# Performance work log

Measured on AMD Instinct MI355X. Metric: run time of the kernel, lower is better.

Reference implementation:

```python
import jax, jax.numpy as jnp
import numpy as np

EPS = 1e-6
K = 20                 # k-NN neighbors (init default)
NEG_SLOPE_CONV = 0.2   # VNLinearLeakyReLU negative_slope in conv_pos / actvn_c
NEG_SLOPE_BLOCK = 0.0  # VNResnetBlockFC uses VNLeakyReLU(negative_slope=0.0)


def vn_linear(w, x):
    # w: [O, C], x: [B, C, 3, ...] -> [B, O, 3, ...]
    return jnp.einsum('oc,bc...->bo...', w, x)


def vn_leaky(x, d, slope):
    # Vector-neuron leaky ReLU: project onto learned direction d per channel.
    dot = jnp.sum(x * d, axis=2, keepdims=True)          # sum over 3-vector dim
    dsq = jnp.sum(d * d, axis=2, keepdims=True)
    x_neg = x - (dot / (dsq + EPS)) * d
    return slope * x + (1.0 - slope) * jnp.where(dot >= 0, x, x_neg)


def vn_lin_leaky(wf, wd, x, slope):
    return vn_leaky(vn_linear(wf, x), vn_linear(wd, x), slope)


def knn_idx(pts, k):
    # pts: [B, N, 3]; largest of negative squared distance = nearest (incl. self)
    d2 = jnp.sum(pts * pts, axis=-1)
    score = 2.0 * jnp.einsum('bnd,bmd->bnm', pts, pts) - d2[:, :, None] - d2[:, None, :]
    _, idx = jax.lax.top_k(score, k)
    return idx                                           # [B, N, k]


def graph_feature_cross(p, k):
    # p: [B, N, 3] -> edge features [B, 3(ch: rel, center, cross), 3(vec), N, k]
    idx = knn_idx(p, k)
    nb = jax.vmap(lambda pts, ix: pts[ix])(p, idx)       # [B, N, k, 3] gather
    ctr = jnp.broadcast_to(p[:, :, None, :], nb.shape)
    cross = jnp.cross(nb, ctr)
    feat = jnp.stack([nb - ctr, ctr, cross], axis=3)     # [B, N, k, 3ch, 3vec]
    return jnp.transpose(feat, (0, 3, 4, 1, 2))


def vn_resnet_block(x, wd0, wf0, wd1, wf1, wsc):
    net = vn_linear(wf0, vn_leaky(x, vn_linear(wd0, x), NEG_SLOPE_BLOCK))
    dx = vn_linear(wf1, vn_leaky(net, vn_linear(wd1, net), NEG_SLOPE_BLOCK))
    return vn_linear(wsc, x) + dx


def setup_inputs() -> dict:
    key = jax.random.key(0)
    ks = jax.random.split(key, 11)
    B, N = 4, 2048
    c_dim, hd = 128, 128
    s = lambda k_, sh, fan: (jax.random.normal(k_, sh, jnp.float32) / np.sqrt(fan).astype(np.float32))
    return {
        'p': jax.random.normal(ks[0], (B, N, 3), jnp.float32),
        'w_conv_feat': s(ks[1], (128, 3), 3),
        'w_conv_dir': s(ks[2], (128, 3), 3),
        'w_fc_pos': s(ks[3], (2 * hd, 128), 128),
        'blk_dir0': s(ks[4], (5, 2 * hd, 2 * hd), 2 * hd),
        'blk_fc0': s(ks[5], (5, hd, 2 * hd), 2 * hd),
        'blk_dir1': s(ks[6], (5, hd, hd), hd),
        'blk_fc1': s(ks[7], (5, hd, hd), hd),
        'blk_sc': s(ks[8], (5, hd, 2 * hd), 2 * hd),
        'w_actc_dir': s(ks[9], (hd, hd), hd),
        'w_fc_c': s(ks[10], (c_dim, hd), hd),
    }


def reference(p, w_conv_feat, w_conv_dir, w_fc_pos, blk_dir0, blk_fc0,
              blk_dir1, blk_fc1, blk_sc, w_actc_dir, w_fc_c):
    feat = graph_feature_cross(p, K)                     # [B, 3, 3, N, K]
    net = vn_lin_leaky(w_conv_feat, w_conv_dir, feat, NEG_SLOPE_CONV)
    net = net.mean(axis=-1)                              # pool over k -> [B,128,3,N]
    net = vn_linear(w_fc_pos, net)                       # [B,256,3,N]
    net = vn_resnet_block(net, blk_dir0[0], blk_fc0[0], blk_dir1[0], blk_fc1[0], blk_sc[0])
    for i in range(1, 5):                                # fixed 5-block stack
        pooled = jnp.broadcast_to(net.mean(axis=-1, keepdims=True), net.shape)
        net = jnp.concatenate([net, pooled], axis=1)     # [B,256,3,N]
        net = vn_resnet_block(net, blk_dir0[i], blk_fc0[i], blk_dir1[i], blk_fc1[i], blk_sc[i])
    net = net.mean(axis=-1)                              # global pool -> [B,128,3]
    net = vn_leaky(net, vn_linear(w_actc_dir, net), NEG_SLOPE_CONV)
    return vn_linear(w_fc_c, net)                        # c: [B,128,3]
```

## Files before the change

### kernel.cpp

```cpp
#include <hip/hip_runtime.h>
#include <math.h>

#define NPT 2048
#define BB 4
#define KNN 20
#define EPSV 1e-6f

typedef unsigned short u16;
typedef unsigned int u32;
typedef _Float16 half8 __attribute__((ext_vector_type(8)));
typedef __attribute__((ext_vector_type(4))) float f32x4;
typedef __attribute__((ext_vector_type(4))) u32 uint4v;

#define MFMAH(a,b,c) __builtin_amdgcn_mfma_f32_16x16x32_f16((a),(b),(c),0,0,0)

__device__ __forceinline__ u16 f2h(float f) {
    _Float16 h = (_Float16)f;
    return __builtin_bit_cast(u16, h);
}
__device__ __forceinline__ float h2f(u16 b) {
    return (float)__builtin_bit_cast(_Float16, b);
}

__global__ __launch_bounds__(256)
// ... 134 lines not shown
            a2 += 0.2f*fz + 0.8f*gz;
        }
        if (kh == 1) { part[o*3+0] = a0; part[o*3+1] = a1; part[o*3+2] = a2; }
        __syncthreads();
        if (kh == 0) {
            a0 += part[o*3+0]; a1 += part[o*3+1]; a2 += part[o*3+2];
            const float s = 1.f / (float)KNN;
            net1[(size_t)(b*6144 +          n)*128 + o] = f2h(a0*s);
            net1[(size_t)(b*6144 + 2048  + n)*128 + o] = f2h(a1*s);
            net1[(size_t)(b*6144 + 4096  + n)*128 + o] = f2h(a2*s);
        }
    }
}

template<int O, int C1, int C2, bool POOL, bool BIASED>
__global__ __launch_bounds__(256) void gemm_plain(
    const u16* __restrict__ W1, int ldw1,
    const u16* __restrict__ X1, int sx1,
    const u16* __restrict__ W2, int ldw2,
    const u16* __restrict__ X2, int sx2,
    const float* __restrict__ WscF, const float* __restrict__ PmPrev,
    u16* __restrict__ Y, int sy,
    float* __restrict__ PmOut)
{
    __shared__ __align__(16) char smem[64*132*4];
    __shared__ float pms[128];
    __shared__ float biasS_s[128];
    const int m0 = blockIdx.x * 64;
    const int ob = blockIdx.y * 128;
    const int b   = m0 / 6144;
    const int vec = (m0 % 6144) / 2048;
    const int tid = threadIdx.x;
    const int lane = tid & 63;
    const int wid = __builtin_amdgcn_readfirstlane(tid >> 6);
    const int wr = wid & 1, wc = wid >> 1;
    const int l15 = lane & 15, l4 = lane >> 4;

    if (BIASED) {
        if (tid < 128) pms[tid] = PmPrev[(size_t)(b*128 + tid)*3 + vec];
        __syncthreads();
        if (tid < 128) {
            const float* wrow = WscF + (size_t)tid*256 + 128;
            float s = 0.f;
            #pragma unroll 4
            for (int c = 0; c < 128; ++c) s += wrow[c]*pms[c];
            biasS_s[tid] = s;
        }
        __syncthreads();
    }

    f32x4 acc[4][2];
    #pragma unroll
    for (int io = 0; io < 4; ++io) {
        float bv[4];
        #pragma unroll
        for (int r = 0; r < 4; ++r)
            bv[r] = BIASED ? biasS_s[wr*64 + io*16 + l4*4 + r] : 0.f;
        #pragma unroll
        for (int jc = 0; jc < 2; ++jc)
            #pragma unroll
            for (int r = 0; r < 4; ++r) acc[io][jc][r] = bv[r];
    }

    constexpr int NS = (C1 + C2) / 64;
    auto ldaddr = [&](int st, int u) -> const u16* {
        const bool ph2 = (st >= C1/64);
        const u16* w = ph2 ? W2 : W1; const u16* x = ph2 ? X2 : X1;
        int ldw = ph2 ? ldw2 : ldw1; int sx = ph2 ? sx2 : sx1;
        int cc = (ph2 ? (st - C1/64) : st) * 64;
        if (u < 1024) {
            int row = u >> 3, q = u & 7;
            return w + (size_t)(ob + row)*ldw + cc + q*8;
        }
        int uu = u - 1024;
        int row = uu >> 3, q = uu & 7;
        return x + (size_t)(m0 + row)*sx + cc + q*8;
    };
    auto lds_dst = [&](int u) -> char* {
        if (u < 1024) { int row = u >> 3, q = u & 7; return smem + row*144 + q*16; }
        int uu = u - 1024;
        int row = uu >> 3, q = uu & 7;
        return smem + 18432 + row*144 + q*16;
    };

    uint4v pf[6];
    #pragma unroll
    for (int j = 0; j < 6; ++j) pf[j] = *reinterpret_cast<const uint4v*>(ldaddr(0, tid + 256*j));
    #pragma unroll
    for (int j = 0; j < 6; ++j) *reinterpret_cast<uint4v*>(lds_dst(tid + 256*j)) = pf[j];

    for (int st = 0; st < NS; ++st) {
        __syncthreads();
        if (st + 1 < NS) {
            #pragma unroll
            for (int j = 0; j < 6; ++j)
                pf[j] = *reinterpret_cast<const uint4v*>(ldaddr(st+1, tid + 256*j));
        }
        #pragma unroll
        for (int ks = 0; ks < 2; ++ks) {
            half8 fA[4], fB[2];
            #pragma unroll
            for (int io = 0; io < 4; ++io)
                fA[io] = *reinterpret_cast<const half8*>(smem + (wr*64 + io*16 + l15)*144 + ks*64 + l4*16);
            #pragma unroll
            for (int i = 0; i < 2; ++i)
                fB[i] = *reinterpret_cast<const half8*>(smem + 18432 + (wc*32 + i*16 + l15)*144 + ks*64 + l4*16);
            #pragma unroll
            for (int io = 0; io < 4; ++io)
                #pragma unroll
                for (int jc = 0; jc < 2; ++jc)
                    acc[io][jc] = MFMAH(fA[io], fB[jc], acc[io][jc]);
        }
        __syncthreads();
        if (st + 1 < NS) {
            #pragma unroll
            for (int j = 0; j < 6; ++j)
                *reinterpret_cast<uint4v*>(lds_dst(tid + 256*j)) = pf[j];
        }
    }

    float* sd = (float*)smem;
    #pragma unroll
    for (int io = 0; io < 4; ++io)
        #pragma unroll
        for (int jc = 0; jc < 2; ++jc) {
            int jj = wc*32 + jc*16 + l15;
            int orow = wr*64 + io*16 + l4*4;
            *reinterpret_cast<f32x4*>(sd + jj*132 + orow) = acc[io][jc];
        }
    __syncthreads();

    #pragma unroll
    for (int rep = 0; rep < 4; ++rep) {
        int task = tid + 256*rep;
        int oc = task & 15, ml = task >> 4;
        const float* dp = sd + ml*132 + oc*8;
        u32 hw[4];
        #pragma unroll
        for (int e2 = 0; e2 < 4; ++e2)
            hw[e2] = (u32)f2h(dp[2*e2]) | ((u32)f2h(dp[2*e2+1]) << 16);
        *reinterpret_cast<uint4v*>(Y + (size_t)(m0 + ml)*sy + ob + oc*8) =
            (uint4v){hw[0],hw[1],hw[2],hw[3]};
    }

    if (POOL) {
        int o_l = tid & 127, half = tid >> 7;
        float sum = 0.f;
        #pragma unroll 8
        for (int c = 0; c < 32; ++c) sum += sd[(half*32 + c)*132 + o_l];
        atomicAdd(&PmOut[(size_t)(b*128 + o_l)*3 + vec], sum * (1.f/(float)NPT));
    }
}

template<int O, int CIN, bool VIRT>
__global__ __launch_bounds__(256) void gemm_dir(
    const u16* __restrict__ W_, int ldw,
    const u16* __restrict__ X1, int sx,
    const float* __restrict__ WdF, const float* __restrict__ Pm,
    u16* __restrict__ Ov, int so,
    float* __restrict__ PmZero)
{
    __shared__ __align__(16) char smem[96*132*4];
    __shared__ float pmd[384];
    __shared__ float biasD_s[384];
    const int gx = blockIdx.x;
    const int b  = gx >> 6;
    const int n0 = (gx & 63) * 32;
    const int ob = blockIdx.y * 128;
    const int tid = threadIdx.x;
    const int lane = tid & 63;
    const int wid = __builtin_amdgcn_readfirstlane(tid >> 6);
    const int wr = wid & 1, wc = wid >> 1;
    const int l15 = lane & 15, l4 = lane >> 4;

    if (PmZero != nullptr && gx == 0 && blockIdx.y == 0)
        for (int t = tid; t < 1536; t += 256) PmZero[t] = 0.f;

    if (VIRT) {
        for (int t = tid; t < 384; t += 256) pmd[t] = Pm[(size_t)b*384 + t];
        __syncthreads();
        for (int t = tid; t < 384; t += 256) {
            int o_l = t / 3, v = t - o_l*3;
            const float* wrow = WdF + (size_t)(ob + o_l)*256 + 128;
            float s = 0.f;
            #pragma unroll 4
            for (int c = 0; c < 128; ++c) s += wrow[c]*pmd[c*3 + v];
            biasD_s[t] = s;
        }
        __syncthreads();
    }

    f32x4 acc[4][3];
    #pragma unroll
    for (int io = 0; io < 4; ++io)
        #pragma unroll
        for (int jc = 0; jc < 3; ++jc) {
            int v = (wc*48 + jc*16) >> 5;
            #pragma unroll
            for (int r = 0; r < 4; ++r) {
                int o_l = wr*64 + io*16 + l4*4 + r;
                acc[io][jc][r] = VIRT ? biasD_s[o_l*3 + v] : 0.f;
            }
        }

    constexpr int NS = CIN / 64;
    auto ldaddr = [&](int st, int u) -> const u16* {
        int cc = st*64;
        if (u < 1024) {
            int row = u >> 3, q = u & 7;
            return W_ + (size_t)(ob + row)*ldw + cc + q*8;
        }
        int uu = u - 1024;
        int row = uu >> 3, q = uu & 7;
        int m = b*6144 + (row >> 5)*2048 + n0 + (row & 31);
        return X1 + (size_t)m*sx + cc + q*8;
    };
    auto lds_dst = [&](int u) -> char* {
        if (u < 1024) { int row = u >> 3, q = u & 7; return smem + row*144 + q*16; }
        int uu = u - 1024;
        int row = uu >> 3, q = uu & 7;
        return smem + 18432 + row*144 + q*16;
    };

    uint4v pf[7];
    #pragma unroll
    for (int j = 0; j < 7; ++j) pf[j] = *reinterpret_cast<const uint4v*>(ldaddr(0, tid + 256*j));
    #pragma unroll
    for (int j = 0; j < 7; ++j) *reinterpret_cast<uint4v*>(lds_dst(tid + 256*j)) = pf[j];

    for (int st = 0; st < NS; ++st) {
        __syncthreads();
        if (st + 1 < NS) {
            #pragma unroll
            for (int j = 0; j < 7; ++j)
                pf[j] = *reinterpret_cast<const uint4v*>(ldaddr(st+1, tid + 256*j));
        }
        #pragma unroll
        for (int ks = 0; ks < 2; ++ks) {
            half8 fA[4], fB[3];
            #pragma unroll
            for (int io = 0; io < 4; ++io)
                fA[io] = *reinterpret_cast<const half8*>(smem + (wr*64 + io*16 + l15)*144 + ks*64 + l4*16);
            #pragma unroll
            for (int i = 0; i < 3; ++i)
                fB[i] = *reinterpret_cast<const half8*>(smem + 18432 + (wc*48 + i*16 + l15)*144 + ks*64 + l4*16);
            #pragma unroll
            for (int io = 0; io < 4; ++io)
                #pragma unroll
                for (int jc = 0; jc < 3; ++jc)
                    acc[io][jc] = MFMAH(fA[io], fB[jc], acc[io][jc]);
        }
        __syncthreads();
        if (st + 1 < NS) {
            #pragma unroll
            for (int j = 0; j < 7; ++j)
                *reinterpret_cast<uint4v*>(lds_dst(tid + 256*j)) = pf[j];
        }
    }

    float* sd = (float*)smem;
    #pragma unroll
    for (int io = 0; io < 4; ++io)
        #pragma unroll
        for (int jc = 0; jc < 3; ++jc) {
            int jj = wc*48 + jc*16 + l15;
            int orow = wr*64 + io*16 + l4*4;
            *reinterpret_cast<f32x4*>(sd + jj*132 + orow) = acc[io][jc];
        }
    __syncthreads();

    #pragma unroll
    for (int rep = 0; rep < 2; ++rep) {
        int task = tid + 256*rep;
        int oc = task & 15, nl = (task >> 4) & 31;
        float d[3][8], x[3][8];
        #pragma unroll
        for (int v = 0; v < 3; ++v) {
            const float* dp = sd + (v*32 + nl)*132 + oc*8;
            #pragma unroll
            for (int e = 0; e < 8; ++e) d[v][e] = dp[e];
        }
        if (VIRT && ob != 0) {
            #pragma unroll
            for (int e = 0; e < 8; ++e) {
                int c = oc*8 + e;
                #pragma unroll
                for (int v = 0; v < 3; ++v)
                    x[v][e] = Pm[(size_t)(b*128 + c)*3 + v];
            }
        } else {
            #pragma unroll
            for (int v = 0; v < 3; ++v) {
                size_t m = (size_t)(b*6144 + v*2048 + n0 + nl);
                uint4v hx = *reinterpret_cast<const uint4v*>(X1 + m*sx + ob + oc*8);
                #pragma unroll
                for (int w = 0; w < 4; ++w) {
                    x[v][2*w]   = h2f((u16)(hx[w] & 0xffffu));
                    x[v][2*w+1] = h2f((u16)(hx[w] >> 16));
                }
            }
        }
        #pragma unroll
        for (int e = 0; e < 8; ++e) {
            float d0 = d[0][e], d1 = d[1][e], d2 = d[2][e];
            float dot = x[0][e]*d0 + x[1][e]*d1 + x[2][e]*d2;
            float dsq = d0*d0 + d1*d1 + d2*d2;
            float t = dot / (dsq + EPSV);
            if (dot < 0.f) { x[0][e] -= t*d0; x[1][e] -= t*d1; x[2][e] -= t*d2; }
        }
        #pragma unroll
        for (int v = 0; v < 3; ++v) {
            u32 hw[4];
            #pragma unroll
            for (int e2 = 0; e2 < 4; ++e2)
                hw[e2] = (u32)f2h(x[v][2*e2]) | ((u32)f2h(x[v][2*e2+1]) << 16);
            *reinterpret_cast<uint4v*>(Ov + (size_t)(b*6144 + v*2048 + n0 + nl)*so + ob + oc*8) =
                (uint4v){hw[0],hw[1],hw[2],hw[3]};
        }
    }
}

template<int CSC, bool VIRT>
__global__ __launch_bounds__(256) void fused_back(
    const u16* __restrict__ Wf0,
    const u16* __restrict__ Wd,
    const u16* __restrict__ Wf1,
    const u16* __restrict__ Wsc,
    const float* __restrict__ WsF,
    const u16* __restrict__ A_,
    const u16* __restrict__ Xs,
    const float* __restrict__ Pm,
    u16* __restrict__ Y,
    float* __restrict__ PmOut)
{
    __shared__ __align__(16) char smem[77568];
    __shared__ float pms[384];
    __shared__ float biasS_s[384];
    constexpr int T_OFF = 0;
    constexpr int U_OFF = 26112;
    constexpr int SW    = 52224;
    const int gx = blockIdx.x;
    const int b  = gx >> 6;
    const int n0 = (gx & 63) * 32;
    const int tid = threadIdx.x;
    const int lane = tid & 63;
    const int wid = __builtin_amdgcn_readfirstlane(tid >> 6);
    const int wr = wid & 1, wc = wid >> 1;
    const int l15 = lane & 15, l4 = lane >> 4;

    if (VIRT) {
        for (int t = tid; t < 384; t += 256) pms[t] = Pm[(size_t)b*384 + t];
        __syncthreads();
        for (int t = tid; t < 384; t += 256) {
            int o_l = t / 3, v = t - o_l*3;
            const float* wrow = WsF + (size_t)o_l*256 + 128;
            float s = 0.f;
            #pragma unroll 4
            for (int c = 0; c < 128; ++c) s += wrow[c]*pms[c*3 + v];
            biasS_s[t] = s;
        }
        __syncthreads();
    }

    uint4v pf[7];

    {
        f32x4 accT[4][3];
        #pragma unroll
        for (int io = 0; io < 4; ++io)
            #pragma unroll
            for (int jc = 0; jc < 3; ++jc)
                accT[io][jc] = (f32x4){0.f,0.f,0.f,0.f};

        auto ldA = [&](int st, int u) -> const u16* {
            int cc = st*64;
            if (u < 1024) { int row = u >> 3, q = u & 7; return Wf0 + (size_t)row*256 + cc + q*8; }
            int uu = u - 1024;
            int row = uu >> 3, q = uu & 7;
            int m = b*6144 + (row >> 5)*2048 + n0 + (row & 31);
            return A_ + (size_t)m*256 + cc + q*8;
        };
        auto stA = [&](int u) -> char* {
            if (u < 1024) { int row = u >> 3, q = u & 7; return smem + SW + row*144 + q*16; }
            int uu = u - 1024;
            int row = uu >> 3, q = uu & 7;
            return smem + T_OFF + row*144 + q*16;
        };

        #pragma unroll
        for (int j = 0; j < 7; ++j) pf[j] = *reinterpret_cast<const uint4v*>(ldA(0, tid + 256*j));
        #pragma unroll
        for (int j = 0; j < 7; ++j) *reinterpret_cast<uint4v*>(stA(tid + 256*j)) = pf[j];

        for (int st = 0; st < 4; ++st) {
            __syncthreads();
            if (st + 1 < 4) {
                #pragma unroll
                for (int j = 0; j < 7; ++j)
                    pf[j] = *reinterpret_cast<const uint4v*>(ldA(st+1, tid + 256*j));
            }
            #pragma unroll
            for (int ks = 0; ks < 2; ++ks) {
                half8 fA[4], fB[3];
                #pragma unroll
                for (int io = 0; io < 4; ++io)
                    fA[io] = *reinterpret_cast<const half8*>(smem + SW + (wr*64 + io*16 + l15)*144 + ks*64 + l4*16);
                #pragma unroll
                for (int i = 0; i < 3; ++i)
                    fB[i] = *reinterpret_cast<const half8*>(smem + T_OFF + (wc*48 + i*16 + l15)*144 + ks*64 + l4*16);
                #pragma unroll
                for (int io = 0; io < 4; ++io)
                    #pragma unroll
                    for (int jc = 0; jc < 3; ++jc)
                        accT[io][jc] = MFMAH(fA[io], fB[jc], accT[io][jc]);
            }
            __syncthreads();
            if (st + 1 < 4) {
                #pragma unroll
                for (int j = 0; j < 7; ++j)
                    *reinterpret_cast<uint4v*>(stA(tid + 256*j)) = pf[j];
            }
        }

        float* sdT = (float*)(smem + U_OFF);
        #pragma unroll
        for (int io = 0; io < 4; ++io)
            #pragma unroll
            for (int jc = 0; jc < 3; ++jc) {
                int jj = wc*48 + jc*16 + l15;
                int orow = wr*64 + io*16 + l4*4;
                *reinterpret_cast<f32x4*>(sdT + jj*132 + orow) = accT[io][jc];
            }
        __syncthreads();
        #pragma unroll
        for (int rep = 0; rep < 6; ++rep) {
            int task = tid + 256*rep;
            int oc = task & 15, cidx = task >> 4;
            const float* dp = sdT + cidx*132 + oc*8;
            u32 hw[4];
            #pragma unroll
            for (int e2 = 0; e2 < 4; ++e2)
                hw[e2] = (u32)f2h(dp[2*e2]) | ((u32)f2h(dp[2*e2+1]) << 16);
            *reinterpret_cast<uint4v*>(smem + T_OFF + cidx*272 + oc*16) =
                (uint4v){hw[0],hw[1],hw[2],hw[3]};
        }
        __syncthreads();
    }

    f32x4 accD[4][3];
    #pragma unroll
    for (int io = 0; io < 4; ++io)
        #pragma unroll
        for (int jc = 0; jc < 3; ++jc)
            accD[io][jc] = (f32x4){0.f,0.f,0.f,0.f};
    {
        auto ldW = [&](int st, int u) -> const u16* {
            int row = u >> 3, q = u & 7;
            return Wd + (size_t)row*128 + st*64 + q*8;
        };
        #pragma unroll
        for (int j = 0; j < 4; ++j) pf[j] = *reinterpret_cast<const uint4v*>(ldW(0, tid + 256*j));
        #pragma unroll
        for (int j = 0; j < 4; ++j) { int u = tid + 256*j; int row = u >> 3, q = u & 7;
            *reinterpret_cast<uint4v*>(smem + SW + row*144 + q*16) = pf[j]; }

        for (int st = 0; st < 2; ++st) {
            __syncthreads();
            if (st + 1 < 2) {
                #pragma unroll
                for (int j = 0; j < 4; ++j)
                    pf[j] = *reinterpret_cast<const uint4v*>(ldW(st+1, tid + 256*j));
            }
            #pragma unroll
            for (int ks = 0; ks < 2; ++ks) {
                half8 fA[4], fB[3];
                #pragma unroll
                for (int io = 0; io < 4; ++io)
                    fA[io] = *reinterpret_cast<const half8*>(smem + SW + (wr*64 + io*16 + l15)*144 + ks*64 + l4*16);
                #pragma unroll
                for (int i = 0; i < 3; ++i)
                    fB[i] = *reinterpret_cast<const half8*>(smem + T_OFF + (wc*48 + i*16 + l15)*272 + st*128 + ks*64 + l4*16);
                #pragma unroll
                for (int io = 0; io < 4; ++io)
                    #pragma unroll
                    for (int jc = 0; jc < 3; ++jc)
                        accD[io][jc] = MFMAH(fA[io], fB[jc], accD[io][jc]);
            }
            __syncthreads();
            if (st + 1 < 2) {
                #pragma unroll
                for (int j = 0; j < 4; ++j) { int u = tid + 256*j; int row = u >> 3, q = u & 7;
                    *reinterpret_cast<uint4v*>(smem + SW + row*144 + q*16) = pf[j]; }
            }
        }
    }

    {
        float* sdT = (float*)(smem + U_OFF);
        #pragma unroll
        for (int io = 0; io < 4; ++io)
            #pragma unroll
            for (int jc = 0; jc < 3; ++jc) {
                int jj = wc*48 + jc*16 + l15;
                int orow = wr*64 + io*16 + l4*4;
                *reinterpret_cast<f32x4*>(sdT + jj*132 + orow) = accD[io][jc];
            }
        __syncthreads();
        #pragma unroll
        for (int rep = 0; rep < 2; ++rep) {
            int task = tid + 256*rep;
            int oc = task & 15, nl = task >> 4;
            float d[3][8], x[3][8];
            #pragma unroll
            for (int v = 0; v < 3; ++v) {
                const float* dp = sdT + (v*32 + nl)*132 + oc*8;
                #pragma unroll
                for (int e = 0; e < 8; ++e) d[v][e] = dp[e];
                uint4v hx = *reinterpret_cast<const uint4v*>(smem + T_OFF + (v*32 + nl)*272 + oc*16);
                #pragma unroll
                for (int w = 0; w < 4; ++w) {
                    x[v][2*w]   = h2f((u16)(hx[w] & 0xffffu));
                    x[v][2*w+1] = h2f((u16)(hx[w] >> 16));
                }
            }
            #pragma unroll
            for (int e = 0; e < 8; ++e) {
                float d0 = d[0][e], d1 = d[1][e], d2 = d[2][e];
                float dot = x[0][e]*d0 + x[1][e]*d1 + x[2][e]*d2;
                float dsq = d0*d0 + d1*d1 + d2*d2;
                float t = dot / (dsq + EPSV);
                if (dot < 0.f) { x[0][e] -= t*d0; x[1][e] -= t*d1; x[2][e] -= t*d2; }
            }
            #pragma unroll
            for (int v = 0; v < 3; ++v) {
                u32 hw[4];
                #pragma unroll
                for (int e2 = 0; e2 < 4; ++e2)
                    hw[e2] = (u32)f2h(x[v][2*e2]) | ((u32)f2h(x[v][2*e2+1]) << 16);
                *reinterpret_cast<uint4v*>(smem + T_OFF + (v*32 + nl)*272 + oc*16) =
                    (uint4v){hw[0],hw[1],hw[2],hw[3]};
            }
        }
        __syncthreads();
    }

    f32x4 acc2[4][3];
    #pragma unroll
    for (int io = 0; io < 4; ++io)
        #pragma unroll
        for (int jc = 0; jc < 3; ++jc) {
            int v = (wc*48 + jc*16) >> 5;
            #pragma unroll
            for (int r = 0; r < 4; ++r) {
                int o_l = wr*64 + io*16 + l4*4 + r;
                acc2[io][jc][r] = VIRT ? biasS_s[o_l*3 + v] : 0.f;
            }
        }

    constexpr int NS2 = 2 + CSC/64;
    auto ld2 = [&](int st, int u) -> const u16* {
        if (st < 2) {
            int row = u >> 3, q = u & 7;
            return Wf1 + (size_t)row*128 + st*64 + q*8;
        }
        int cc = (st - 2)*64;
        if (u < 1024) { int row = u >> 3, q = u & 7; return Wsc + (size_t)row*256 + cc + q*8; }
        int uu = u - 1024;
        int row = uu >> 3, q = uu & 7;
        int m = b*6144 + (row >> 5)*2048 + n0 + (row & 31);
        return Xs + (size_t)m*CSC + cc + q*8;
    };
    auto st2 = [&](int u) -> char* {
        if (u < 1024) { int row = u >> 3, q = u & 7; return smem + SW + row*144 + q*16; }
        int uu = u - 1024;
        int row = uu >> 3, q = uu & 7;
        return smem + U_OFF + row*144 + q*16;
    };

    #pragma unroll
    for (int j = 0; j < 7; ++j) { int u = tid + 256*j; if (u < 1024) pf[j] = *reinterpret_cast<const uint4v*>(ld2(0, u)); }
    #pragma unroll
    for (int j = 0; j < 7; ++j) { int u = tid + 256*j; if (u < 1024) *reinterpret_cast<uint4v*>(st2(u)) = pf[j]; }

    for (int st = 0; st < NS2; ++st) {
        __syncthreads();
        int nv = (st + 1 < 2) ? 1024 : 1792;
        if (st + 1 < NS2) {
            #pragma unroll
            for (int j = 0; j < 7; ++j) { int u = tid + 256*j; if (u < nv) pf[j] = *reinterpret_cast<const uint4v*>(ld2(st+1, u)); }
        }
        #pragma unroll
        for (int ks = 0; ks < 2; ++ks) {
            half8 fA[4], fB[3];
            #pragma unroll
            for (int io = 0; io < 4; ++io)
                fA[io] = *reinterpret_cast<const half8*>(smem + SW + (wr*64 + io*16 + l15)*144 + ks*64 + l4*16);
            if (st < 2) {
                #pragma unroll
                for (int i = 0; i < 3; ++i)
                    fB[i] = *reinterpret_cast<const half8*>(smem + T_OFF + (wc*48 + i*16 + l15)*272 + st*128 + ks*64 + l4*16);
            } else {
                #pragma unroll
                for (int i = 0; i < 3; ++i)
                    fB[i] = *reinterpret_cast<const half8*>(smem + U_OFF + (wc*48 + i*16 + l15)*144 + ks*64 + l4*16);
            }
            #pragma unroll
            for (int io = 0; io < 4; ++io)
                #pragma unroll
                for (int jc = 0; jc < 3; ++jc)
                    acc2[io][jc] = MFMAH(fA[io], fB[jc], acc2[io][jc]);
        }
        __syncthreads();
        if (st + 1 < NS2) {
            #pragma unroll
            for (int j = 0; j < 7; ++j) { int u = tid + 256*j; if (u < nv) *reinterpret_cast<uint4v*>(st2(u)) = pf[j]; }
        }
    }

    float* sdE = (float*)smem;
    #pragma unroll
    for (int io = 0; io < 4; ++io)
        #pragma unroll
        for (int jc = 0; jc < 3; ++jc) {
            int jj = wc*48 + jc*16 + l15;
            int orow = wr*64 + io*16 + l4*4;
            *reinterpret_cast<f32x4*>(sdE + jj*132 + orow) = acc2[io][jc];
        }
    __syncthreads();
    if (Y != nullptr) {
        #pragma unroll
        for (int rep = 0; rep < 2; ++rep) {
            int task = tid + 256*rep;
            int oc = task & 15, nl = (task >> 4) & 31;
            #pragma unroll
            for (int v = 0; v < 3; ++v) {
                const float* dp = sdE + (v*32 + nl)*132 + oc*8;
                u32 hw[4];
                #pragma unroll
                for (int e2 = 0; e2 < 4; ++e2)
                    hw[e2] = (u32)f2h(dp[2*e2]) | ((u32)f2h(dp[2*e2+1]) << 16);
                *reinterpret_cast<uint4v*>(Y + (size_t)(b*6144 + v*2048 + n0 + nl)*128 + oc*8) =
                    (uint4v){hw[0],hw[1],hw[2],hw[3]};
            }
        }
    }
    for (int t = tid; t < 384; t += 256) {
        int v = t >> 7, o_l = t & 127;
        float sum = 0.f;
        #pragma unroll 8
        for (int nl = 0; nl < 32; ++nl) sum += sdE[(v*32 + nl)*132 + o_l];
        atomicAdd(&PmOut[(size_t)(b*128 + o_l)*3 + v], sum * (1.f/(float)NPT));
    }
}

#define WO_FCPOS 0
#define WO_DIR0  32768
#define WO_FC0   360448
#define WO_DIR1  524288
#define WO_FC1   606208
#define WO_SC    688128
#define WTOT     851968
__global__ __launch_bounds__(256)
void convert_w_kernel(const float* __restrict__ s0, const float* __restrict__ s1,
                      const float* __restrict__ s2, const float* __restrict__ s3,
                      const float* __restrict__ s4, const float* __restrict__ s5,
                      u16* __restrict__ Wf) {
    int t = blockIdx.x*256 + threadIdx.x;
    if (t >= WTOT) return;
    const float* src; int base;
    if      (t < WO_DIR0) { src = s0; base = WO_FCPOS; }
    else if (t < WO_FC0)  { src = s1; base = WO_DIR0; }
    else if (t < WO_DIR1) { src = s2; base = WO_FC0; }
    else if (t < WO_FC1)  { src = s3; base = WO_DIR1; }
    else if (t < WO_SC)   { src = s4; base = WO_FC1; }
    else                  { src = s5; base = WO_SC; }
    Wf[t] = f2h(src[t - base]);
}

__global__ __launch_bounds__(128)
void final_head_kernel(const float* __restrict__ q, const float* __restrict__ Wdir,
                       const float* __restrict__ Wfc, float* __restrict__ out) {
    int b = blockIdx.x; int o = threadIdx.x;
    __shared__ float qs[128][3];
    __shared__ float zs[128][3];
    qs[o][0] = q[((size_t)b*128 + o)*3 + 0];
    qs[o][1] = q[((size_t)b*128 + o)*3 + 1];
    qs[o][2] = q[((size_t)b*128 + o)*3 + 2];
    __syncthreads();
    float d0 = 0.f, d1 = 0.f, d2 = 0.f;
    for (int c = 0; c < 128; ++c) {
        float w = Wdir[o*128 + c];
        d0 += w*qs[c][0]; d1 += w*qs[c][1]; d2 += w*qs[c][2];
    }
    float x0 = qs[o][0], x1 = qs[o][1], x2 = qs[o][2];
    float dot = d0*x0 + d1*x1 + d2*x2;
    float dsq = d0*d0 + d1*d1 + d2*d2;
    float t = dot / (dsq + EPSV);
    bool pos = dot >= 0.f;
    float g0 = pos ? x0 : (x0 - t*d0);
    float g1 = pos ? x1 : (x1 - t*d1);
    float g2 = pos ? x2 : (x2 - t*d2);
    zs[o][0] = 0.2f*x0 + 0.8f*g0;
    zs[o][1] = 0.2f*x1 + 0.8f*g1;
    zs[o][2] = 0.2f*x2 + 0.8f*g2;
    __syncthreads();
    float c0 = 0.f, c1 = 0.f, c2 = 0.f;
    for (int c = 0; c < 128; ++c) {
        float w = Wfc[o*128 + c];
        c0 += w*zs[c][0]; c1 += w*zs[c][1]; c2 += w*zs[c][2];
    }
    out[((size_t)b*128 + o)*3 + 0] = c0;
    out[((size_t)b*128 + o)*3 + 1] = c1;
    out[((size_t)b*128 + o)*3 + 2] = c2;
}

extern "C" void kernel_launch(void* const* d_in, const int* in_sizes, int n_in,
                              void* d_out, int out_size, void* d_ws, size_t ws_size,
                              hipStream_t stream) {
    const float* p           = (const float*)d_in[0];
    const float* w_conv_feat = (const float*)d_in[1];
    const float* w_conv_dir  = (const float*)d_in[2];
    const float* w_fc_pos    = (const float*)d_in[3];
    const float* blk_dir0    = (const float*)d_in[4];
    const float* blk_fc0     = (const float*)d_in[5];
    const float* blk_dir1    = (const float*)d_in[6];
    const float* blk_fc1     = (const float*)d_in[7];
    const float* blk_sc      = (const float*)d_in[8];
    const float* w_actc_dir  = (const float*)d_in[9];
    const float* w_fc_c      = (const float*)d_in[10];
    float* out = (float*)d_out;

    char* wsb = (char*)d_ws;
    size_t cur = 0;
    auto carve = [&](size_t nbytes) -> char* {
        char* r = wsb + cur;
        cur += (nbytes + 255) & ~(size_t)255;
        return r;
    };
    const size_t MTOT = (size_t)BB*3*NPT;
    float* Pm0   = (float*)carve(1536*4);
    float* Pm1   = (float*)carve(1536*4);
    u16* Wf    = (u16*)carve((size_t)WTOT*2);
    u16* net1  = (u16*)carve(MTOT*128*2);
    u16* X0    = (u16*)carve(MTOT*256*2);
    u16* Ab    = (u16*)carve(MTOT*256*2);
    u16* Yb    = (u16*)carve(MTOT*128*2);
    float* PmBuf[2] = { Pm0, Pm1 };

    convert_w_kernel<<<(WTOT+255)/256, 256, 0, stream>>>(
        w_fc_pos, blk_dir0, blk_fc0, blk_dir1, blk_fc1, blk_sc, Wf);
    knn_edge_kernel<<<BB*NPT, 256, 0, stream>>>(p, w_conv_feat, w_conv_dir, net1);

    gemm_plain<256,128,0,false,false><<<dim3(384,2), 256, 0, stream>>>(
        Wf+WO_FCPOS, 128, net1, 128,
        nullptr, 0, nullptr, 0,
        nullptr, nullptr, X0, 256, nullptr);

    const u16* Yp = nullptr;
    for (int i = 0; i < 5; ++i) {
        size_t od0 = WO_DIR0 + (size_t)i*65536;
        size_t of0 = WO_FC0  + (size_t)i*32768;
        size_t od1 = WO_DIR1 + (size_t)i*16384;
        size_t of1 = WO_FC1  + (size_t)i*16384;
        size_t osc = WO_SC   + (size_t)i*32768;
        float* PmPrev = PmBuf[(i+1) & 1];
        float* PmCur  = PmBuf[i & 1];

        if (i == 0) {
            gemm_dir<256,256,false><<<dim3(BB*64,2), 256, 0, stream>>>(
                Wf+od0, 256, X0, 256, nullptr, nullptr, Ab, 256, PmCur);
        } else {
            gemm_dir<256,128,true><<<dim3(BB*64,2), 256, 0, stream>>>(
                Wf+od0, 256, Yp, 128,
                blk_dir0 + (size_t)i*65536, PmPrev, Ab, 256, PmCur);
        }

        u16* outv = (i == 4) ? nullptr : ((i % 2 == 0) ? Yb : X0);
        if (i == 0) {
            fused_back<256,false><<<BB*64, 256, 0, stream>>>(
                Wf+of0, Wf+od1, Wf+of1, Wf+osc, nullptr,
                Ab, X0, nullptr, outv, PmCur);
        } else {
            fused_back<128,true><<<BB*64, 256, 0, stream>>>(
                Wf+of0, Wf+od1, Wf+of1, Wf+osc, blk_sc + (size_t)i*32768,
                Ab, Yp, PmPrev, outv, PmCur);
        }
        Yp = outv;
    }

    final_head_kernel<<<BB, 128, 0, stream>>>(PmBuf[0], w_actc_dir, w_fc_c, out);
}
```

Baseline: 288.6 us.

## Fuse direction GEMM and leaky ReLU into per-block resnet kernel

Result: slower. 311.3 us (+7.9%).

```diff
diff --git a/kernel.cpp b/kernel.cpp
--- a/kernel.cpp
+++ b/kernel.cpp
@@ -310,193 +310,28 @@
     }
 }
 
-template<int O, int CIN, bool VIRT>
-__global__ __launch_bounds__(256) void gemm_dir(
-    const u16* __restrict__ W_, int ldw,
-    const u16* __restrict__ X1, int sx,
-    const float* __restrict__ WdF, const float* __restrict__ Pm,
-    u16* __restrict__ Ov, int so,
-    float* __restrict__ PmZero)
-{
-    __shared__ __align__(16) char smem[96*132*4];
-    __shared__ float pmd[384];
-    __shared__ float biasD_s[384];
-    const int gx = blockIdx.x;
-    const int b  = gx >> 6;
-    const int n0 = (gx & 63) * 32;
-    const int ob = blockIdx.y * 128;
-    const int tid = threadIdx.x;
-    const int lane = tid & 63;
-    const int wid = __builtin_amdgcn_readfirstlane(tid >> 6);
-    const int wr = wid & 1, wc = wid >> 1;
-    const int l15 = lane & 15, l4 = lane >> 4;
-
-    if (PmZero != nullptr && gx == 0 && blockIdx.y == 0)
-        for (int t = tid; t < 1536; t += 256) PmZero[t] = 0.f;
-
-    if (VIRT) {
-        for (int t = tid; t < 384; t += 256) pmd[t] = Pm[(size_t)b*384 + t];
-        __syncthreads();
-        for (int t = tid; t < 384; t += 256) {
-            int o_l = t / 3, v = t - o_l*3;
-            const float* wrow = WdF + (size_t)(ob + o_l)*256 + 128;
-            float s = 0.f;
-            #pragma unroll 4
-            for (int c = 0; c < 128; ++c) s += wrow[c]*pmd[c*3 + v];
-            biasD_s[t] = s;
-        }
-        __syncthreads();
-    }
-
-    f32x4 acc[4][3];
-    #pragma unroll
-    for (int io = 0; io < 4; ++io)
-        #pragma unroll
-        for (int jc = 0; jc < 3; ++jc) {
-            int v = (wc*48 + jc*16) >> 5;
-            #pragma unroll
-            for (int r = 0; r < 4; ++r) {
-                int o_l = wr*64 + io*16 + l4*4 + r;
-                acc[io][jc][r] = VIRT ? biasD_s[o_l*3 + v] : 0.f;
-            }
-        }
-
-    constexpr int NS = CIN / 64;
-    auto ldaddr = [&](int st, int u) -> const u16* {
-        int cc = st*64;
-        if (u < 1024) {
-            int row = u >> 3, q = u & 7;
-            return W_ + (size_t)(ob + row)*ldw + cc + q*8;
-        }
-        int uu = u - 1024;
-        int row = uu >> 3, q = uu & 7;
-        int m = b*6144 + (row >> 5)*2048 + n0 + (row & 31);
-        return X1 + (size_t)m*sx + cc + q*8;
-    };
-    auto lds_dst = [&](int u) -> char* {
-        if (u < 1024) { int row = u >> 3, q = u & 7; return smem + row*144 + q*16; }
-        int uu = u - 1024;
-        int row = uu >> 3, q = uu & 7;
-        return smem + 18432 + row*144 + q*16;
-    };
-
-    uint4v pf[7];
-    #pragma unroll
-    for (int j = 0; j < 7; ++j) pf[j] = *reinterpret_cast<const uint4v*>(ldaddr(0, tid + 256*j));
-    #pragma unroll
-    for (int j = 0; j < 7; ++j) *reinterpret_cast<uint4v*>(lds_dst(tid + 256*j)) = pf[j];
-
-    for (int st = 0; st < NS; ++st) {
-        __syncthreads();
-        if (st + 1 < NS) {
-            #pragma unroll
-            for (int j = 0; j < 7; ++j)
-                pf[j] = *reinterpret_cast<const uint4v*>(ldaddr(st+1, tid + 256*j));
-        }
-        #pragma unroll
-        for (int ks = 0; ks < 2; ++ks) {
-            half8 fA[4], fB[3];
-            #pragma unroll
-            for (int io = 0; io < 4; ++io)
-                fA[io] = *reinterpret_cast<const half8*>(smem + (wr*64 + io*16 + l15)*144 + ks*64 + l4*16);
-            #pragma unroll
-            for (int i = 0; i < 3; ++i)
-                fB[i] = *reinterpret_cast<const half8*>(smem + 18432 + (wc*48 + i*16 + l15)*144 + ks*64 + l4*16);
-            #pragma unroll
-            for (int io = 0; io < 4; ++io)
-                #pragma unroll
-                for (int jc = 0; jc < 3; ++jc)
-                    acc[io][jc] = MFMAH(fA[io], fB[jc], acc[io][jc]);
-        }
-        __syncthreads();
-        if (st + 1 < NS) {
-            #pragma unroll
-            for (int j = 0; j < 7; ++j)
-                *reinterpret_cast<uint4v*>(lds_dst(tid + 256*j)) = pf[j];
-        }
-    }
-
-    float* sd = (float*)smem;
-    #pragma unroll
-    for (int io = 0; io < 4; ++io)
-        #pragma unroll
-        for (int jc = 0; jc < 3; ++jc) {
-            int jj = wc*48 + jc*16 + l15;
-            int orow = wr*64 + io*16 + l4*4;
-            *reinterpret_cast<f32x4*>(sd + jj*132 + orow) = acc[io][jc];
-        }
-    __syncthreads();
-
-    #pragma unroll
-    for (int rep = 0; rep < 2; ++rep) {
-        int task = tid + 256*rep;
-        int oc = task & 15, nl = (task >> 4) & 31;
-        float d[3][8], x[3][8];
-        #pragma unroll
-        for (int v = 0; v < 3; ++v) {
-            const float* dp = sd + (v*32 + nl)*132 + oc*8;
-            #pragma unroll
-            for (int e = 0; e < 8; ++e) d[v][e] = dp[e];
-        }
-        if (VIRT && ob != 0) {
-            #pragma unroll
-            for (int e = 0; e < 8; ++e) {
-                int c = oc*8 + e;
-                #pragma unroll
-                for (int v = 0; v < 3; ++v)
-                    x[v][e] = Pm[(size_t)(b*128 + c)*3 + v];
-            }
-        } else {
-            #pragma unroll
-            for (int v = 0; v < 3; ++v) {
-                size_t m = (size_t)(b*6144 + v*2048 + n0 + nl);
-                uint4v hx = *reinterpret_cast<const uint4v*>(X1 + m*sx + ob + oc*8);
-                #pragma unroll
-                for (int w = 0; w < 4; ++w) {
-                    x[v][2*w]   = h2f((u16)(hx[w] & 0xffffu));
-                    x[v][2*w+1] = h2f((u16)(hx[w] >> 16));
-                }
-            }
-        }
-        #pragma unroll
-        for (int e = 0; e < 8; ++e) {
-            float d0 = d[0][e], d1 = d[1][e], d2 = d[2][e];
-            float dot = x[0][e]*d0 + x[1][e]*d1 + x[2][e]*d2;
-            float dsq = d0*d0 + d1*d1 + d2*d2;
-            float t = dot / (dsq + EPSV);
-            if (dot < 0.f) { x[0][e] -= t*d0; x[1][e] -= t*d1; x[2][e] -= t*d2; }
-        }
-        #pragma unroll
-        for (int v = 0; v < 3; ++v) {
-            u32 hw[4];
-            #pragma unroll
-            for (int e2 = 0; e2 < 4; ++e2)
-                hw[e2] = (u32)f2h(x[v][2*e2]) | ((u32)f2h(x[v][2*e2+1]) << 16);
-            *reinterpret_cast<uint4v*>(Ov + (size_t)(b*6144 + v*2048 + n0 + nl)*so + ob + oc*8) =
-                (uint4v){hw[0],hw[1],hw[2],hw[3]};
-        }
-    }
-}
-
-template<int CSC, bool VIRT>
-__global__ __launch_bounds__(256) void fused_back(
+template<int CIN, bool VIRT>
+__global__ __launch_bounds__(256) void fused_iter(
+    const u16* __restrict__ Wd0,
+    const float* __restrict__ Wd0F,
     const u16* __restrict__ Wf0,
-    const u16* __restrict__ Wd,
+    const u16* __restrict__ Wd1,
     const u16* __restrict__ Wf1,
     const u16* __restrict__ Wsc,
     const float* __restrict__ WsF,
-    const u16* __restrict__ A_,
-    const u16* __restrict__ Xs,
+    const u16* __restrict__ Xin,
     const float* __restrict__ Pm,
     u16* __restrict__ Y,
     float* __restrict__ PmOut)
 {
-    __shared__ __align__(16) char smem[77568];
+    __shared__ __align__(16) char smem[76800];
     __shared__ float pms[384];
     __shared__ float biasS_s[384];
-    constexpr int T_OFF = 0;
-    constexpr int U_OFF = 26112;
-    constexpr int SW    = 52224;
+    __shared__ float biasD_s[384];
+    constexpr int R0  = 0;
+    constexpr int R1  = 26112;
+    constexpr int WST = R1;
+    constexpr int XST = R1 + 18432;
     const int gx = blockIdx.x;
     const int b  = gx >> 6;
     const int n0 = (gx & 63) * 32;
@@ -521,66 +356,198 @@
     }
 
     uint4v pf[7];
-
-    {
-        f32x4 accT[4][3];
+    f32x4 accT[4][3];
+    #pragma unroll
+    for (int io = 0; io < 4; ++io)
+        #pragma unroll
+        for (int jc = 0; jc < 3; ++jc)
+            accT[io][jc] = (f32x4){0.f,0.f,0.f,0.f};
+
+    for (int h = 0; h < 2; ++h) {
+        if (VIRT) {
+            __syncthreads();
+            for (int t = tid; t < 384; t += 256) {
+                int o_l = t / 3, v = t - o_l*3;
+                const float* wrow = Wd0F + (size_t)(h*128 + o_l)*256 + 128;
+                float s = 0.f;
+                #pragma unroll 4
+                for (int c = 0; c < 128; ++c) s += wrow[c]*pms[c*3 + v];
+                biasD_s[t] = s;
+            }
+            __syncthreads();
+        }
+
+        f32x4 accD0[4][3];
         #pragma unroll
         for (int io = 0; io < 4; ++io)
             #pragma unroll
-            for (int jc = 0; jc < 3; ++jc)
-                accT[io][jc] = (f32x4){0.f,0.f,0.f,0.f};
-
-        auto ldA = [&](int st, int u) -> const u16* {
+            for (int jc = 0; jc < 3; ++jc) {
+                int v = (wc*48 + jc*16) >> 5;
+                #pragma unroll
+                for (int r = 0; r < 4; ++r) {
+                    int o_l = wr*64 + io*16 + l4*4 + r;
+                    accD0[io][jc][r] = VIRT ? biasD_s[o_l*3 + v] : 0.f;
+                }
+            }
+
+        auto ldD = [&](int st, int u) -> const u16* {
             int cc = st*64;
-            if (u < 1024) { int row = u >> 3, q = u & 7; return Wf0 + (size_t)row*256 + cc + q*8; }
+            if (u < 1024) { int row = u >> 3, q = u & 7;
+                return Wd0 + (size_t)(h*128 + row)*256 + cc + q*8; }
             int uu = u - 1024;
             int row = uu >> 3, q = uu & 7;
             int m = b*6144 + (row >> 5)*2048 + n0 + (row & 31);
-            return A_ + (size_t)m*256 + cc + q*8;
+            return Xin + (size_t)m*CIN + cc + q*8;
         };
-        auto stA = [&](int u) -> char* {
-            if (u < 1024) { int row = u >> 3, q = u & 7; return smem + SW + row*144 + q*16; }
+        auto stD = [&](int u) -> char* {
+            if (u < 1024) { int row = u >> 3, q = u & 7; return smem + WST + row*144 + q*16; }
             int uu = u - 1024;
             int row = uu >> 3, q = uu & 7;
-            return smem + T_OFF + row*144 + q*16;
+            return smem + XST + row*144 + q*16;
         };
-
-        #pragma unroll
-        for (int j = 0; j < 7; ++j) pf[j] = *reinterpret_cast<const uint4v*>(ldA(0, tid + 256*j));
-        #pragma unroll
-        for (int j = 0; j < 7; ++j) *reinterpret_cast<uint4v*>(stA(tid + 256*j)) = pf[j];
-
-        for (int st = 0; st < 4; ++st) {
+        constexpr int NSD = CIN / 64;
+        #pragma unroll
+        for (int j = 0; j < 7; ++j) pf[j] = *reinterpret_cast<const uint4v*>(ldD(0, tid + 256*j));
+        #pragma unroll
+        for (int j = 0; j < 7; ++j) *reinterpret_cast<uint4v*>(stD(tid + 256*j)) = pf[j];
+        for (int st = 0; st < NSD; ++st) {
             __syncthreads();
-            if (st + 1 < 4) {
+            if (st + 1 < NSD) {
                 #pragma unroll
                 for (int j = 0; j < 7; ++j)
-                    pf[j] = *reinterpret_cast<const uint4v*>(ldA(st+1, tid + 256*j));
+                    pf[j] = *reinterpret_cast<const uint4v*>(ldD(st+1, tid + 256*j));
             }
             #pragma unroll
             for (int ks = 0; ks < 2; ++ks) {
                 half8 fA[4], fB[3];
                 #pragma unroll
                 for (int io = 0; io < 4; ++io)
-                    fA[io] = *reinterpret_cast<const half8*>(smem + SW + (wr*64 + io*16 + l15)*144 + ks*64 + l4*16);
+                    fA[io] = *reinterpret_cast<const half8*>(smem + WST + (wr*64 + io*16 + l15)*144 + ks*64 + l4*16);
                 #pragma unroll
                 for (int i = 0; i < 3; ++i)
-                    fB[i] = *reinterpret_cast<const half8*>(smem + T_OFF + (wc*48 + i*16 + l15)*144 + ks*64 + l4*16);
+                    fB[i] = *reinterpret_cast<const half8*>(smem + XST + (wc*48 + i*16 + l15)*144 + ks*64 + l4*16);
                 #pragma unroll
                 for (int io = 0; io < 4; ++io)
                     #pragma unroll
                     for (int jc = 0; jc < 3; ++jc)
-                        accT[io][jc] = MFMAH(fA[io], fB[jc], accT[io][jc]);
+                        accD0[io][jc] = MFMAH(fA[io], fB[jc], accD0[io][jc]);
             }
             __syncthreads();
-            if (st + 1 < 4) {
+            if (st + 1 < NSD) {
                 #pragma unroll
                 for (int j = 0; j < 7; ++j)
-                    *reinterpret_cast<uint4v*>(stA(tid + 256*j)) = pf[j];
-            }
-        }
-
-        float* sdT = (float*)(smem + U_OFF);
+                    *reinterpret_cast<uint4v*>(stD(tid + 256*j)) = pf[j];
+            }
+        }
+
+        {
+            float* sd = (float*)(smem + R1);
+            #pragma unroll
+            for (int io = 0; io < 4; ++io)
+                #pragma unroll
+                for (int jc = 0; jc < 3; ++jc) {
+                    int jj = wc*48 + jc*16 + l15;
+                    int orow = wr*64 + io*16 + l4*4;
+                    *reinterpret_cast<f32x4*>(sd + jj*132 + orow) = accD0[io][jc];
+                }
+            __syncthreads();
+            #pragma unroll
+            for (int rep = 0; rep < 2; ++rep) {
+                int task = tid + 256*rep;
+                int oc = task & 15, nl = task >> 4;
+                float d[3][8], x[3][8];
+                #pragma unroll
+                for (int v = 0; v < 3; ++v) {
+                    const float* dp = sd + (v*32 + nl)*132 + oc*8;
+                    #pragma unroll
+                    for (int e = 0; e < 8; ++e) d[v][e] = dp[e];
+                }
+                if (VIRT && h == 1) {
+                    #pragma unroll
+                    for (int e = 0; e < 8; ++e) {
+                        int c = oc*8 + e;
+                        #pragma unroll
+                        for (int v = 0; v < 3; ++v)
+                            x[v][e] = pms[c*3 + v];
+                    }
+                } else {
+                    #pragma unroll
+                    for (int v = 0; v < 3; ++v) {
+                        size_t m = (size_t)(b*6144 + v*2048 + n0 + nl);
+                        uint4v hx = *reinterpret_cast<const uint4v*>(
+                            Xin + m*CIN + (VIRT ? 0 : h*128) + oc*8);
+                        #pragma unroll
+                        for (int w = 0; w < 4; ++w) {
+                            x[v][2*w]   = h2f((u16)(hx[w] & 0xffffu));
+                            x[v][2*w+1] = h2f((u16)(hx[w] >> 16));
+                        }
+                    }
+                }
+                #pragma unroll
+                for (int e = 0; e < 8; ++e) {
+                    float d0 = d[0][e], d1 = d[1][e], d2 = d[2][e];
+                    float dot = x[0][e]*d0 + x[1][e]*d1 + x[2][e]*d2;
+                    float dsq = d0*d0 + d1*d1 + d2*d2;
+                    float t = dot / (dsq + EPSV);
+                    if (dot < 0.f) { x[0][e] -= t*d0; x[1][e] -= t*d1; x[2][e] -= t*d2; }
+                }
+                #pragma unroll
+                for (int v = 0; v < 3; ++v) {
+                    u32 hw[4];
+                    #pragma unroll
+                    for (int e2 = 0; e2 < 4; ++e2)
+                        hw[e2] = (u32)f2h(x[v][2*e2]) | ((u32)f2h(x[v][2*e2+1]) << 16);
+                    *reinterpret_cast<uint4v*>(smem + R0 + (v*32 + nl)*272 + oc*16) =
+                        (uint4v){hw[0],hw[1],hw[2],hw[3]};
+                }
+            }
+            __syncthreads();
+        }
+
+        {
+            auto ldF0 = [&](int st, int u) -> const u16* {
+                int row = u >> 3, q = u & 7;
+                return Wf0 + (size_t)row*256 + h*128 + st*64 + q*8;
+            };
+            #pragma unroll
+            for (int j = 0; j < 4; ++j) pf[j] = *reinterpret_cast<const uint4v*>(ldF0(0, tid + 256*j));
+            #pragma unroll
+            for (int j = 0; j < 4; ++j) { int u = tid + 256*j; int row = u >> 3, q = u & 7;
+                *reinterpret_cast<uint4v*>(smem + WST + row*144 + q*16) = pf[j]; }
+            for (int st = 0; st < 2; ++st) {
+                __syncthreads();
+                if (st + 1 < 2) {
+                    #pragma unroll
+                    for (int j = 0; j < 4; ++j)
+                        pf[j] = *reinterpret_cast<const uint4v*>(ldF0(st+1, tid + 256*j));
+                }
+                #pragma unroll
+                for (int ks = 0; ks < 2; ++ks) {
+                    half8 fA[4], fB[3];
+                    #pragma unroll
+                    for (int io = 0; io < 4; ++io)
+                        fA[io] = *reinterpret_cast<const half8*>(smem + WST + (wr*64 + io*16 + l15)*144 + ks*64 + l4*16);
+                    #pragma unroll
+                    for (int i = 0; i < 3; ++i)
+                        fB[i] = *reinterpret_cast<const half8*>(smem + R0 + (wc*48 + i*16 + l15)*272 + st*128 + ks*64 + l4*16);
+                    #pragma unroll
+                    for (int io = 0; io < 4; ++io)
+                        #pragma unroll
+                        for (int jc = 0; jc < 3; ++jc)
+                            accT[io][jc] = MFMAH(fA[io], fB[jc], accT[io][jc]);
+                }
+                __syncthreads();
+                if (st + 1 < 2) {
+                    #pragma unroll
+                    for (int j = 0; j < 4; ++j) { int u = tid + 256*j; int row = u >> 3, q = u & 7;
+                        *reinterpret_cast<uint4v*>(smem + WST + row*144 + q*16) = pf[j]; }
+                }
+            }
+        }
+    }
+
+    {
+        float* sdT = (float*)(smem + R1);
         #pragma unroll
         for (int io = 0; io < 4; ++io)
             #pragma unroll
@@ -599,7 +566,7 @@
             #pragma unroll
             for (int e2 = 0; e2 < 4; ++e2)
                 hw[e2] = (u32)f2h(dp[2*e2]) | ((u32)f2h(dp[2*e2+1]) << 16);
-            *reinterpret_cast<uint4v*>(smem + T_OFF + cidx*272 + oc*16) =
+            *reinterpret_cast<uint4v*>(smem + R0 + cidx*272 + oc*16) =
                 (uint4v){hw[0],hw[1],hw[2],hw[3]};
         }
         __syncthreads();
@@ -614,14 +581,13 @@
     {
         auto ldW = [&](int st, int u) -> const u16* {
             int row = u >> 3, q = u & 7;
-            return Wd + (size_t)row*128 + st*64 + q*8;
+            return Wd1 + (size_t)row*128 + st*64 + q*8;
         };
         #pragma unroll
         for (int j = 0; j < 4; ++j) pf[j] = *reinterpret_cast<const uint4v*>(ldW(0, tid + 256*j));
         #pragma unroll
         for (int j = 0; j < 4; ++j) { int u = tid + 256*j; int row = u >> 3, q = u & 7;
-            *reinterpret_cast<uint4v*>(smem + SW + row*144 + q*16) = pf[j]; }
-
+            *reinterpret_cast<uint4v*>(smem + WST + row*144 + q*16) = pf[j]; }
         for (int st = 0; st < 2; ++st) {
             __syncthreads();
             if (st + 1 < 2) {
@@ -634,10 +600,10 @@
                 half8 fA[4], fB[3];
                 #pragma unroll
                 for (int io = 0; io < 4; ++io)
-                    fA[io] = *reinterpret_cast<const half8*>(smem + SW + (wr*64 + io*16 + l15)*144 + ks*64 + l4*16);
+                    fA[io] = *reinterpret_cast<const half8*>(smem + WST + (wr*64 + io*16 + l15)*144 + ks*64 + l4*16);
                 #pragma unroll
                 for (int i = 0; i < 3; ++i)
-                    fB[i] = *reinterpret_cast<const half8*>(smem + T_OFF + (wc*48 + i*16 + l15)*272 + st*128 + ks*64 + l4*16);
+                    fB[i] = *reinterpret_cast<const half8*>(smem + R0 + (wc*48 + i*16 + l15)*272 + st*128 + ks*64 + l4*16);
                 #pragma unroll
                 for (int io = 0; io < 4; ++io)
                     #pragma unroll
@@ -648,13 +614,13 @@
             if (st + 1 < 2) {
                 #pragma unroll
                 for (int j = 0; j < 4; ++j) { int u = tid + 256*j; int row = u >> 3, q = u & 7;
-                    *reinterpret_cast<uint4v*>(smem + SW + row*144 + q*16) = pf[j]; }
+                    *reinterpret_cast<uint4v*>(smem + WST + row*144 + q*16) = pf[j]; }
             }
         }
     }
 
     {
-        float* sdT = (float*)(smem + U_OFF);
+        float* sdT = (float*)(smem + R1);
         #pragma unroll
         for (int io = 0; io < 4; ++io)
             #pragma unroll
@@ -674,7 +640,7 @@
                 const float* dp = sdT + (v*32 + nl)*132 + oc*8;
                 #pragma unroll
                 for (int e = 0; e < 8; ++e) d[v][e] = dp[e];
-                uint4v hx = *reinterpret_cast<const uint4v*>(smem + T_OFF + (v*32 + nl)*272 + oc*16);
+                uint4v hx = *reinterpret_cast<const uint4v*>(smem + R0 + (v*32 + nl)*272 + oc*16);
                 #pragma unroll
                 for (int w = 0; w < 4; ++w) {
                     x[v][2*w]   = h2f((u16)(hx[w] & 0xffffu));
@@ -695,7 +661,7 @@
                 #pragma unroll
                 for (int e2 = 0; e2 < 4; ++e2)
                     hw[e2] = (u32)f2h(x[v][2*e2]) | ((u32)f2h(x[v][2*e2+1]) << 16);
-                *reinterpret_cast<uint4v*>(smem + T_OFF + (v*32 + nl)*272 + oc*16) =
+                *reinterpret_cast<uint4v*>(smem + R0 + (v*32 + nl)*272 + oc*16) =
                     (uint4v){hw[0],hw[1],hw[2],hw[3]};
             }
         }
@@ -715,7 +681,7 @@
             }
         }
 
-    constexpr int NS2 = 2 + CSC/64;
+    constexpr int NS2 = 2 + CIN/64;
     auto ld2 = [&](int st, int u) -> const u16* {
         if (st < 2) {
             int row = u >> 3, q = u & 7;
@@ -726,13 +692,13 @@
         int uu = u - 1024;
         int row = uu >> 3, q = uu & 7;
         int m = b*6144 + (row >> 5)*2048 + n0 + (row & 31);
-        return Xs + (size_t)m*CSC + cc + q*8;
+        return Xin + (size_t)m*CIN + cc + q*8;
     };
     auto st2 = [&](int u) -> char* {
-        if (u < 1024) { int row = u >> 3, q = u & 7; return smem + SW + row*144 + q*16; }
+        if (u < 1024) { int row = u >> 3, q = u & 7; return smem + WST + row*144 + q*16; }
         int uu = u - 1024;
         int row = uu >> 3, q = uu & 7;
-        return smem + U_OFF + row*144 + q*16;
+        return smem + XST + row*144 + q*16;
     };
 
     #pragma unroll
@@ -752,15 +718,15 @@
             half8 fA[4], fB[3];
             #pragma unroll
             for (int io = 0; io < 4; ++io)
-                fA[io] = *reinterpret_cast<const half8*>(smem + SW + (wr*64 + io*16 + l15)*144 + ks*64 + l4*16);
+                fA[io] = *reinterpret_cast<const half8*>(smem + WST + (wr*64 + io*16 + l15)*144 + ks*64 + l4*16);
             if (st < 2) {
                 #pragma unroll
                 for (int i = 0; i < 3; ++i)
-                    fB[i] = *reinterpret_cast<const half8*>(smem + T_OFF + (wc*48 + i*16 + l15)*272 + st*128 + ks*64 + l4*16);
+                    fB[i] = *reinterpret_cast<const half8*>(smem + R0 + (wc*48 + i*16 + l15)*272 + st*128 + ks*64 + l4*16);
             } else {
                 #pragma unroll
                 for (int i = 0; i < 3; ++i)
-                    fB[i] = *reinterpret_cast<const half8*>(smem + U_OFF + (wc*48 + i*16 + l15)*144 + ks*64 + l4*16);
+                    fB[i] = *reinterpret_cast<const half8*>(smem + XST + (wc*48 + i*16 + l15)*144 + ks*64 + l4*16);
             }
             #pragma unroll
             for (int io = 0; io < 4; ++io)
@@ -775,7 +741,7 @@
         }
     }
 
-    float* sdE = (float*)smem;
+    float* sdE = (float*)(smem + R1);
     #pragma unroll
     for (int io = 0; io < 4; ++io)
         #pragma unroll
@@ -822,9 +788,10 @@
 void convert_w_kernel(const float* __restrict__ s0, const float* __restrict__ s1,
                       const float* __restrict__ s2, const float* __restrict__ s3,
                       const float* __restrict__ s4, const float* __restrict__ s5,
-                      u16* __restrict__ Wf) {
+                      u16* __restrict__ Wf, float* __restrict__ PmAll) {
     int t = blockIdx.x*256 + threadIdx.x;
     if (t >= WTOT) return;
+    if (t < 5*1536) PmAll[t] = 0.f;
     const float* src; int base;
     if      (t < WO_DIR0) { src = s0; base = WO_FCPOS; }
     else if (t < WO_FC0)  { src = s1; base = WO_DIR0; }
@@ -896,17 +863,13 @@
         return r;
     };
     const size_t MTOT = (size_t)BB*3*NPT;
-    float* Pm0   = (float*)carve(1536*4);
-    float* Pm1   = (float*)carve(1536*4);
+    float* PmAll = (float*)carve(5*1536*4);
     u16* Wf    = (u16*)carve((size_t)WTOT*2);
     u16* net1  = (u16*)carve(MTOT*128*2);
     u16* X0    = (u16*)carve(MTOT*256*2);
-    u16* Ab    = (u16*)carve(MTOT*256*2);
     u16* Yb    = (u16*)carve(MTOT*128*2);
-    float* PmBuf[2] = { Pm0, Pm1 };
-
     convert_w_kernel<<<(WTOT+255)/256, 256, 0, stream>>>(
-        w_fc_pos, blk_dir0, blk_fc0, blk_dir1, blk_fc1, blk_sc, Wf);
+        w_fc_pos, blk_dir0, blk_fc0, blk_dir1, blk_fc1, blk_sc, Wf, PmAll);
     knn_edge_kernel<<<BB*NPT, 256, 0, stream>>>(p, w_conv_feat, w_conv_dir, net1);
 
     gemm_plain<256,128,0,false,false><<<dim3(384,2), 256, 0, stream>>>(
@@ -921,30 +884,22 @@
         size_t od1 = WO_DIR1 + (size_t)i*16384;
         size_t of1 = WO_FC1  + (size_t)i*16384;
         size_t osc = WO_SC   + (size_t)i*32768;
-        float* PmPrev = PmBuf[(i+1) & 1];
-        float* PmCur  = PmBuf[i & 1];
-
-        if (i == 0) {
-            gemm_dir<256,256,false><<<dim3(BB*64,2), 256, 0, stream>>>(
-                Wf+od0, 256, X0, 256, nullptr, nullptr, Ab, 256, PmCur);
-        } else {
-            gemm_dir<256,128,true><<<dim3(BB*64,2), 256, 0, stream>>>(
-                Wf+od0, 256, Yp, 128,
-                blk_dir0 + (size_t)i*65536, PmPrev, Ab, 256, PmCur);
-        }
+        float* PmPrev = (i == 0) ? nullptr : (PmAll + (size_t)(i-1)*1536);
+        float* PmCur  = PmAll + (size_t)i*1536;
 
         u16* outv = (i == 4) ? nullptr : ((i % 2 == 0) ? Yb : X0);
         if (i == 0) {
-            fused_back<256,false><<<BB*64, 256, 0, stream>>>(
-                Wf+of0, Wf+od1, Wf+of1, Wf+osc, nullptr,
-                Ab, X0, nullptr, outv, PmCur);
+            fused_iter<256,false><<<BB*64, 256, 0, stream>>>(
+                Wf+od0, nullptr, Wf+of0, Wf+od1, Wf+of1, Wf+osc, nullptr,
+                X0, nullptr, outv, PmCur);
         } else {
-            fused_back<128,true><<<BB*64, 256, 0, stream>>>(
-                Wf+of0, Wf+od1, Wf+of1, Wf+osc, blk_sc + (size_t)i*32768,
-                Ab, Yp, PmPrev, outv, PmCur);
+            fused_iter<128,true><<<BB*64, 256, 0, stream>>>(
+                Wf+od0, blk_dir0 + (size_t)i*65536, Wf+of0, Wf+od1, Wf+of1,
+                Wf+osc, blk_sc + (size_t)i*32768,
+                Yp, PmPrev, outv, PmCur);
         }
         Yp = outv;
     }
 
-    final_head_kernel<<<BB, 128, 0, stream>>>(PmBuf[0], w_actc_dir, w_fc_c, out);
+    final_head_kernel<<<BB, 128, 0, stream>>>(PmAll + 4*1536, w_actc_dir, w_fc_c, out);
 }
```
